# Performance work log

Measured on AMD Instinct MI355X. Metric: run time of the kernel, lower is better.

The kernel has to match this reference:

```python
import jax, jax.numpy as jnp
import numpy as np

D = 20                 # input_dim
N = 1_000_000          # batch
NC = 2 ** (D + 1)      # number of dummy expert Linear(1,1) modules


def setup_inputs() -> dict:
    key = jax.random.key(0)
    ks = jax.random.split(key, 12)
    x = jax.random.randint(ks[0], (N, D), 0, 2).astype(jnp.float32)   # binary features
    t = jax.random.randint(ks[1], (N, 1), 0, 2).astype(jnp.float32)   # binary treatment
    y = jax.random.normal(ks[2], (N, 1), dtype=jnp.float32)           # outcome fed to dummy linears
    # Encoder dummy experts: one (w, b) pair per combination of (t, x)
    qz_w = jax.random.normal(ks[3], (NC,), dtype=jnp.float32) * 0.1
    qz_b = jax.random.normal(ks[4], (NC,), dtype=jnp.float32) * 0.1
    # Decoder per-feature Linear(1,1) for binary x
    dx_w = jax.random.normal(ks[5], (D,), dtype=jnp.float32) * 0.1
    dx_b = jax.random.normal(ks[6], (D,), dtype=jnp.float32) * 0.1
    # Decoder scalar Linear(1,1) heads
    t_w = jax.random.normal(ks[7], (), dtype=jnp.float32) * 0.1
    t_b = jnp.zeros((), jnp.float32)
    y0_w = jax.random.normal(ks[8], (), dtype=jnp.float32) * 0.1
    y0_b = jnp.zeros((), jnp.float32)
    y1_w = jax.random.normal(ks[9], (), dtype=jnp.float32) * 0.1
    y1_b = jnp.zeros((), jnp.float32)
    pz_logit = jnp.zeros((1,), jnp.float32)
    return {"x": x, "t": t, "y": y, "qz_w": qz_w, "qz_b": qz_b,
            "dx_w": dx_w, "dx_b": dx_b, "t_w": t_w, "t_b": t_b,
            "y0_w": y0_w, "y0_b": y0_b, "y1_w": y1_w, "y1_b": y1_b,
            "pz_logit": pz_logit}


def _combo_index(x, t):
    # itertools.product([0,1], repeat=D+1): combs[i][0] is the t bit (MSB),
    # combs[i][1:] are the x bits, so i = t*2^D + sum_j x_j * 2^(D-1-j).
    pow2 = (2 ** jnp.arange(D - 1, -1, -1)).astype(jnp.int32)   # [D]
    return t[:, 0].astype(jnp.int32) * (2 ** D) + x.astype(jnp.int32) @ pow2  # [N]


def _decode(z, t, dx_w, dx_b, t_w, t_b, y0_w, y0_b, y1_w, y1_b):
    # Vectorized form of per-feature Linear(1,1) loops: x_logits[:, i] = w_i*z + b_i
    x_logits = z * dx_w[None, :] + dx_b[None, :]          # [N, D]
    t_logits = z * t_w + t_b                              # [N, 1]
    y_logits = (z * y1_w + y1_b) * t + (z * y0_w + y0_b) * (1.0 - t)  # [N, 1]
    return x_logits, t_logits, y_logits


def reference(x, t, y, qz_w, qz_b, dx_w, dx_b, t_w, t_b,
              y0_w, y0_b, y1_w, y1_b, pz_logit):
    # Encoder (z_mode='binary'): sum over all 2^(D+1) experts of
    # (w_i*y + b_i) * onehot_mask_i == gather by combination index (inputs binary).
    idx = _combo_index(x, t)                                  # [N]
    z_logits = (qz_w[idx] * y[:, 0] + qz_b[idx])[:, None]     # [N, 1]
    n = x.shape[0]
    z0 = jnp.zeros((n, 1), jnp.float32)
    z1 = jnp.ones((n, 1), jnp.float32)
    x_logits0, t_logits0, y_logits0 = _decode(z0, t, dx_w, dx_b, t_w, t_b, y0_w, y0_b, y1_w, y1_b)
    x_logits1, t_logits1, y_logits1 = _decode(z1, t, dx_w, dx_b, t_w, t_b, y0_w, y0_b, y1_w, y1_b)
    return (z_logits, x_logits0, x_logits1, t_logits0, t_logits1,
            y_logits0, y_logits1, pz_logit)
```

## Files before the change

### kernel.cpp

```cpp
#include <hip/hip_runtime.h>

constexpr int D = 20;

typedef float f4 __attribute__((ext_vector_type(4)));
typedef unsigned int u32;

__device__ __forceinline__ u32 bf16_rne(float f) {
    u32 u = __float_as_uint(f);
    return (u + 0x7FFFu + ((u >> 16) & 1u)) >> 16;
}

__global__ __launch_bounds__(256) void cevae_build_tab(
    const f4* __restrict__ qw, const f4* __restrict__ qb,
    uint4* __restrict__ tab, int nq)
{
    int i = blockIdx.x * 256 + threadIdx.x;
    if (i >= nq) return;
    f4 w = qw[i];
    f4 b = qb[i];
    uint4 o;
    o.x = (bf16_rne(w.x) << 16) | bf16_rne(b.x);
    o.y = (bf16_rne(w.y) << 16) | bf16_rne(b.y);
    o.z = (bf16_rne(w.z) << 16) | bf16_rne(b.z);
    o.w = (bf16_rne(w.w) << 16) | bf16_rne(b.w);
    tab[i] = o;
}

template <bool USE_TAB>
__global__ __launch_bounds__(256) void cevae_fused6_kernel(
    const float* __restrict__ x, const float* __restrict__ t,
    const float* __restrict__ y, const u32* __restrict__ tab,
    const float* __restrict__ qz_w, const float* __restrict__ qz_b,
    const float* __restrict__ dx_w, const float* __restrict__ dx_b,
    const float* __restrict__ sc_tw, const float* __restrict__ sc_tb,
    const float* __restrict__ sc_y0w, const float* __restrict__ sc_y0b,
    const float* __restrict__ sc_y1w, const float* __restrict__ sc_y1b,
    const float* __restrict__ pz, float* __restrict__ out, int n_rows,
    int n_job_blocks)
{
    int bid = blockIdx.x;
    int sub = ((bid >> 4) << 3) | (bid & 7);
    size_t o3 = (size_t)n_rows * (size_t)(1 + 2 * D);

    if (((bid >> 3) & 1) == 0) {
        int n = sub * 256 + threadIdx.x;
        if (n >= n_rows) return;

        const f4* xr = (const f4*)(x + (size_t)n * D);
        f4 a = xr[0];
        f4 b = xr[1];
        f4 c = xr[2];
        f4 d = xr[3];
        f4 e = xr[4];
        float tv = t[n];
        float yv = y[n];

        unsigned idx = (tv != 0.0f) ? (1u << 20) : 0u;
        idx |= ((unsigned)a.x) << 19;
        idx |= ((unsigned)a.y) << 18;
        idx |= ((unsigned)a.z) << 17;
        idx |= ((unsigned)a.w) << 16;
        idx |= ((unsigned)b.x) << 15;
        idx |= ((unsigned)b.y) << 14;
        idx |= ((unsigned)b.z) << 13;
        idx |= ((unsigned)b.w) << 12;
        idx |= ((unsigned)c.x) << 11;
        idx |= ((unsigned)c.y) << 10;
        idx |= ((unsigned)c.z) << 9;
        idx |= ((unsigned)c.w) << 8;
        idx |= ((unsigned)d.x) << 7;
        idx |= ((unsigned)d.y) << 6;
        idx |= ((unsigned)d.z) << 5;
        idx |= ((unsigned)d.w) << 4;
        idx |= ((unsigned)e.x) << 3;
        idx |= ((unsigned)e.y) << 2;
        idx |= ((unsigned)e.z) << 1;
        idx |= ((unsigned)e.w);

        float z;
        if (USE_TAB) {
            u32 g = tab[idx];
            z = fmaf(__uint_as_float(g & 0xFFFF0000u), yv,
                     __uint_as_float(g << 16));
        } else {
            z = fmaf(qz_w[idx], yv, qz_b[idx]);
        }
        out[n] = z;

        float y0w = *sc_y0w, y0b = *sc_y0b;
        float y1w = *sc_y1w, y1b = *sc_y1b;

        out[o3 + 2 * (size_t)n_rows + n] = fmaf(tv, y1b - y0b, y0b);
        out[o3 + 3 * (size_t)n_rows + n] = fmaf(tv, (y1w + y1b) - (y0w + y0b), y0w + y0b);
        if (n == 0) out[o3 + 4 * (size_t)n_rows] = pz[0];
    } else {
        unsigned Q = (unsigned)n_rows * D / 4;
        f4* r0 = (f4*)(out + n_rows);
        f4* r1 = r0 + Q;
        unsigned stride = (unsigned)n_job_blocks * 256;
        unsigned q0 = (unsigned)sub * 256 + threadIdx.x;
        for (unsigned q = q0; q < Q; q += stride) {
            int cb = (int)(q % 5u) * 4;
            float b0 = dx_b[cb + 0], b1 = dx_b[cb + 1];
            float b2 = dx_b[cb + 2], b3 = dx_b[cb + 3];
            float w0 = dx_w[cb + 0], w1 = dx_w[cb + 1];
            float w2 = dx_w[cb + 2], w3 = dx_w[cb + 3];
            f4 v0 = {b0, b1, b2, b3};
            f4 v1 = {w0 + b0, w1 + b1, w2 + b2, w3 + b3};
            r0[q] = v0;
            r1[q] = v1;
        }
        float tw = *sc_tw, tb = *sc_tb;
        f4 s0 = {tb, tb, tb, tb};
        float t1v = tw + tb;
        f4 s1 = {t1v, t1v, t1v, t1v};
        unsigned Qt = (unsigned)n_rows / 4;
        f4* h0 = (f4*)(out + o3);
        f4* h1 = (f4*)(out + o3 + (size_t)n_rows);
        for (unsigned q = q0; q < Qt; q += stride) {
            h0[q] = s0;
            h1[q] = s1;
        }
    }
}

extern "C" void kernel_launch(void* const* d_in, const int* in_sizes, int n_in,
                              void* d_out, int out_size, void* d_ws, size_t ws_size,
                              hipStream_t stream) {
    const float* x    = (const float*)d_in[0];
    const float* t    = (const float*)d_in[1];
    const float* y    = (const float*)d_in[2];
    const float* qz_w = (const float*)d_in[3];
    const float* qz_b = (const float*)d_in[4];
    const float* dx_w = (const float*)d_in[5];
    const float* dx_b = (const float*)d_in[6];
    const float* t_w  = (const float*)d_in[7];
    const float* t_b  = (const float*)d_in[8];
    const float* y0_w = (const float*)d_in[9];
    const float* y0_b = (const float*)d_in[10];
    const float* y1_w = (const float*)d_in[11];
    const float* y1_b = (const float*)d_in[12];
    const float* pz   = (const float*)d_in[13];
    float* out = (float*)d_out;

    int n_rows = in_sizes[0] / D;
    int nc     = in_sizes[3];
    int n_rb = (n_rows + 255) / 256;
    int n_groups = (n_rb + 7) / 8;
    int n_job_blocks = n_groups * 8;

    size_t tab_bytes = (size_t)nc * sizeof(u32);
    if (ws_size >= tab_bytes) {
        uint4* tab = (uint4*)d_ws;
        int nq = nc / 4;
        cevae_build_tab<<<(nq + 255) / 256, 256, 0, stream>>>(
            (const f4*)qz_w, (const f4*)qz_b, tab, nq);
        cevae_fused6_kernel<true><<<n_groups * 16, 256, 0, stream>>>(
            x, t, y, (const u32*)tab, qz_w, qz_b, dx_w, dx_b, t_w, t_b,
            y0_w, y0_b, y1_w, y1_b, pz, out, n_rows, n_job_blocks);
    } else {
        cevae_fused6_kernel<false><<<n_groups * 16, 256, 0, stream>>>(
            x, t, y, nullptr, qz_w, qz_b, dx_w, dx_b, t_w, t_b,
            y0_w, y0_b, y1_w, y1_b, pz, out, n_rows, n_job_blocks);
    }
}
```

Baseline: 75.56 us.

## Fuse table build with constant fill, run row gather in separate kernel

Moves the write-only fill of the decoder logits and t heads out of the row kernel and into the table-build kernel, which gets 4096 extra blocks. The row kernel becomes a plain one-row-per-thread gather. The large constant fill now overlaps with the small table build, rather than sharing blocks with the gather. The work is still two launches, and the fill no longer runs alongside the gather's memory traffic, so the overall schedule may not improve.

```diff
diff --git a/kernel.cpp b/kernel.cpp
--- a/kernel.cpp
+++ b/kernel.cpp
@@ -10,95 +10,33 @@
     return (u + 0x7FFFu + ((u >> 16) & 1u)) >> 16;
 }
 
-__global__ __launch_bounds__(256) void cevae_build_tab(
+__global__ __launch_bounds__(256) void cevae_A_build_fill(
     const f4* __restrict__ qw, const f4* __restrict__ qb,
-    uint4* __restrict__ tab, int nq)
-{
-    int i = blockIdx.x * 256 + threadIdx.x;
-    if (i >= nq) return;
-    f4 w = qw[i];
-    f4 b = qb[i];
-    uint4 o;
-    o.x = (bf16_rne(w.x) << 16) | bf16_rne(b.x);
-    o.y = (bf16_rne(w.y) << 16) | bf16_rne(b.y);
-    o.z = (bf16_rne(w.z) << 16) | bf16_rne(b.z);
-    o.w = (bf16_rne(w.w) << 16) | bf16_rne(b.w);
-    tab[i] = o;
-}
-
-template <bool USE_TAB>
-__global__ __launch_bounds__(256) void cevae_fused6_kernel(
-    const float* __restrict__ x, const float* __restrict__ t,
-    const float* __restrict__ y, const u32* __restrict__ tab,
-    const float* __restrict__ qz_w, const float* __restrict__ qz_b,
+    uint4* __restrict__ tab, int nq,
     const float* __restrict__ dx_w, const float* __restrict__ dx_b,
     const float* __restrict__ sc_tw, const float* __restrict__ sc_tb,
-    const float* __restrict__ sc_y0w, const float* __restrict__ sc_y0b,
-    const float* __restrict__ sc_y1w, const float* __restrict__ sc_y1b,
-    const float* __restrict__ pz, float* __restrict__ out, int n_rows,
-    int n_job_blocks)
+    float* __restrict__ out, int n_rows,
+    int n_build_blocks, int n_fill_blocks)
 {
     int bid = blockIdx.x;
-    int sub = ((bid >> 4) << 3) | (bid & 7);
-    size_t o3 = (size_t)n_rows * (size_t)(1 + 2 * D);
-
-    if (((bid >> 3) & 1) == 0) {
-        int n = sub * 256 + threadIdx.x;
-        if (n >= n_rows) return;
-
-        const f4* xr = (const f4*)(x + (size_t)n * D);
-        f4 a = xr[0];
-        f4 b = xr[1];
-        f4 c = xr[2];
-        f4 d = xr[3];
-        f4 e = xr[4];
-        float tv = t[n];
-        float yv = y[n];
-
-        unsigned idx = (tv != 0.0f) ? (1u << 20) : 0u;
-        idx |= ((unsigned)a.x) << 19;
-        idx |= ((unsigned)a.y) << 18;
-        idx |= ((unsigned)a.z) << 17;
-        idx |= ((unsigned)a.w) << 16;
-        idx |= ((unsigned)b.x) << 15;
-        idx |= ((unsigned)b.y) << 14;
-        idx |= ((unsigned)b.z) << 13;
-        idx |= ((unsigned)b.w) << 12;
-        idx |= ((unsigned)c.x) << 11;
-        idx |= ((unsigned)c.y) << 10;
-        idx |= ((unsigned)c.z) << 9;
-        idx |= ((unsigned)c.w) << 8;
-        idx |= ((unsigned)d.x) << 7;
-        idx |= ((unsigned)d.y) << 6;
-        idx |= ((unsigned)d.z) << 5;
-        idx |= ((unsigned)d.w) << 4;
-        idx |= ((unsigned)e.x) << 3;
-        idx |= ((unsigned)e.y) << 2;
-        idx |= ((unsigned)e.z) << 1;
-        idx |= ((unsigned)e.w);
-
-        float z;
-        if (USE_TAB) {
-            u32 g = tab[idx];
-            z = fmaf(__uint_as_float(g & 0xFFFF0000u), yv,
-                     __uint_as_float(g << 16));
-        } else {
-            z = fmaf(qz_w[idx], yv, qz_b[idx]);
-        }
-        out[n] = z;
-
-        float y0w = *sc_y0w, y0b = *sc_y0b;
-        float y1w = *sc_y1w, y1b = *sc_y1b;
-
-        out[o3 + 2 * (size_t)n_rows + n] = fmaf(tv, y1b - y0b, y0b);
-        out[o3 + 3 * (size_t)n_rows + n] = fmaf(tv, (y1w + y1b) - (y0w + y0b), y0w + y0b);
-        if (n == 0) out[o3 + 4 * (size_t)n_rows] = pz[0];
+    if (bid < n_build_blocks) {
+        int i = bid * 256 + threadIdx.x;
+        if (i >= nq) return;
+        f4 w = qw[i];
+        f4 b = qb[i];
+        uint4 o;
+        o.x = (bf16_rne(w.x) << 16) | bf16_rne(b.x);
+        o.y = (bf16_rne(w.y) << 16) | bf16_rne(b.y);
+        o.z = (bf16_rne(w.z) << 16) | bf16_rne(b.z);
+        o.w = (bf16_rne(w.w) << 16) | bf16_rne(b.w);
+        tab[i] = o;
     } else {
+        int fb = bid - n_build_blocks;
         unsigned Q = (unsigned)n_rows * D / 4;
         f4* r0 = (f4*)(out + n_rows);
         f4* r1 = r0 + Q;
-        unsigned stride = (unsigned)n_job_blocks * 256;
-        unsigned q0 = (unsigned)sub * 256 + threadIdx.x;
+        unsigned stride = (unsigned)n_fill_blocks * 256;
+        unsigned q0 = (unsigned)fb * 256 + threadIdx.x;
         for (unsigned q = q0; q < Q; q += stride) {
             int cb = (int)(q % 5u) * 4;
             float b0 = dx_b[cb + 0], b1 = dx_b[cb + 1];
@@ -114,6 +52,7 @@
         f4 s0 = {tb, tb, tb, tb};
         float t1v = tw + tb;
         f4 s1 = {t1v, t1v, t1v, t1v};
+        size_t o3 = (size_t)n_rows * (size_t)(1 + 2 * D);
         unsigned Qt = (unsigned)n_rows / 4;
         f4* h0 = (f4*)(out + o3);
         f4* h1 = (f4*)(out + o3 + (size_t)n_rows);
@@ -122,6 +61,68 @@
             h1[q] = s1;
         }
     }
+}
+
+template <bool USE_TAB>
+__global__ __launch_bounds__(256) void cevae_B_rows(
+    const float* __restrict__ x, const float* __restrict__ t,
+    const float* __restrict__ y, const u32* __restrict__ tab,
+    const float* __restrict__ qz_w, const float* __restrict__ qz_b,
+    const float* __restrict__ sc_y0w, const float* __restrict__ sc_y0b,
+    const float* __restrict__ sc_y1w, const float* __restrict__ sc_y1b,
+    const float* __restrict__ pz, float* __restrict__ out, int n_rows)
+{
+    int n = blockIdx.x * 256 + threadIdx.x;
+    if (n >= n_rows) return;
+
+    const f4* xr = (const f4*)(x + (size_t)n * D);
+    f4 a = xr[0];
+    f4 b = xr[1];
+    f4 c = xr[2];
+    f4 d = xr[3];
+    f4 e = xr[4];
+    float tv = t[n];
+    float yv = y[n];
+
+    unsigned idx = (tv != 0.0f) ? (1u << 20) : 0u;
+    idx |= ((unsigned)a.x) << 19;
+    idx |= ((unsigned)a.y) << 18;
+    idx |= ((unsigned)a.z) << 17;
+    idx |= ((unsigned)a.w) << 16;
+    idx |= ((unsigned)b.x) << 15;
+    idx |= ((unsigned)b.y) << 14;
+    idx |= ((unsigned)b.z) << 13;
+    idx |= ((unsigned)b.w) << 12;
+    idx |= ((unsigned)c.x) << 11;
+    idx |= ((unsigned)c.y) << 10;
+    idx |= ((unsigned)c.z) << 9;
+    idx |= ((unsigned)c.w) << 8;
+    idx |= ((unsigned)d.x) << 7;
+    idx |= ((unsigned)d.y) << 6;
+    idx |= ((unsigned)d.z) << 5;
+    idx |= ((unsigned)d.w) << 4;
+    idx |= ((unsigned)e.x) << 3;
+    idx |= ((unsigned)e.y) << 2;
+    idx |= ((unsigned)e.z) << 1;
+    idx |= ((unsigned)e.w);
+
+    float z;
+    if (USE_TAB) {
+        u32 g = tab[idx];
+        z = fmaf(__uint_as_float(g & 0xFFFF0000u), yv,
+                 __uint_as_float(g << 16));
+    } else {
+        z = fmaf(qz_w[idx], yv, qz_b[idx]);
+    }
+    out[n] = z;
+
+    float y0w = *sc_y0w, y0b = *sc_y0b;
+    float y1w = *sc_y1w, y1b = *sc_y1b;
+
+    size_t o3 = (size_t)n_rows * (size_t)(1 + 2 * D);
+    out[o3 + 2 * (size_t)n_rows + n] = fmaf(tv, y1b - y0b, y0b);
+    out[o3 + 3 * (size_t)n_rows + n] = fmaf(tv, (y1w + y1b) - (y0w + y0b), y0w + y0b);
+    if (n == 0) out[o3 + 4 * (size_t)n_rows] = pz[0];
 }
 
 extern "C" void kernel_launch(void* const* d_in, const int* in_sizes, int n_in,
@@ -146,21 +147,25 @@
     int n_rows = in_sizes[0] / D;
     int nc     = in_sizes[3];
     int n_rb = (n_rows + 255) / 256;
-    int n_groups = (n_rb + 7) / 8;
-    int n_job_blocks = n_groups * 8;
 
     size_t tab_bytes = (size_t)nc * sizeof(u32);
     if (ws_size >= tab_bytes) {
         uint4* tab = (uint4*)d_ws;
         int nq = nc / 4;
-        cevae_build_tab<<<(nq + 255) / 256, 256, 0, stream>>>(
-            (const f4*)qz_w, (const f4*)qz_b, tab, nq);
-        cevae_fused6_kernel<true><<<n_groups * 16, 256, 0, stream>>>(
-            x, t, y, (const u32*)tab, qz_w, qz_b, dx_w, dx_b, t_w, t_b,
-            y0_w, y0_b, y1_w, y1_b, pz, out, n_rows, n_job_blocks);
+        int n_build_blocks = (nq + 255) / 256;
+        int n_fill_blocks  = 4096;
+        cevae_A_build_fill<<<n_build_blocks + n_fill_blocks, 256, 0, stream>>>(
+            (const f4*)qz_w, (const f4*)qz_b, tab, nq,
+            dx_w, dx_b, t_w, t_b, out, n_rows, n_build_blocks, n_fill_blocks);
+        cevae_B_rows<true><<<n_rb, 256, 0, stream>>>(
+            x, t, y, (const u32*)tab, qz_w, qz_b,
+            y0_w, y0_b, y1_w, y1_b, pz, out, n_rows);
     } else {
-        cevae_fused6_kernel<false><<<n_groups * 16, 256, 0, stream>>>(
-            x, t, y, nullptr, qz_w, qz_b, dx_w, dx_b, t_w, t_b,
-            y0_w, y0_b, y1_w, y1_b, pz, out, n_rows, n_job_blocks);
+        cevae_A_build_fill<<<4096, 256, 0, stream>>>(
+            (const f4*)qz_w, (const f4*)qz_b, nullptr, 0,
+            dx_w, dx_b, t_w, t_b, out, n_rows, 0, 4096);
+        cevae_B_rows<false><<<n_rb, 256, 0, stream>>>(
+            x, t, y, nullptr, qz_w, qz_b,
+            y0_w, y0_b, y1_w, y1_b, pz, out, n_rows);
     }
 }
```

Result: faster. 67.52 us (-10.6%).
